# Optimization experiments

Hardware: AMD Instinct MI355X
Metric: run time of the kernel (lower is better)

## Reference

```python
import jax, jax.numpy as jnp
import numpy as np

T, H, I, E, K = 1024, 2048, 1408, 8, 2  # tokens, hidden, moe_intermediate, n_experts, top_k

def setup_inputs() -> dict:
    key = jax.random.key(0)
    k0, k1, k2, k3 = jax.random.split(key, 4)
    def w(k, shape, fan_in):
        return jax.random.normal(k, shape, jnp.float32) / np.float32(np.sqrt(fan_in))
    return {
        "hidden_states": jax.random.normal(k0, (T, H), jnp.float32),
        "gate_w": w(k1, (H, E), H),      # router: LiteLinear(H -> E), no bias
        "w1": w(k2, (E, H, I), H),        # experts_w1 [E, H, I]
        "w2": w(k3, (E, I, H), I),        # experts_w2 [E, I, H]
    }

def reference(hidden_states, gate_w, w1, w2):
    # Router: logits -> softmax -> top-k expert probabilities (no renorm; Qwen2MoE norm_topk_prob=False)
    router_logits = hidden_states @ gate_w                      # [T, E]
    probs = jax.nn.softmax(router_logits, axis=-1)              # [T, E]
    topk_vals, topk_idx = jax.lax.top_k(probs, K)               # [T, K]
    # Dense combine weights: zero except at the top-k experts of each token
    combine = jnp.sum(jax.nn.one_hot(topk_idx, E, dtype=probs.dtype) * topk_vals[..., None], axis=1)  # [T, E]
    # Expert MLP per source: down(silu(x @ w1)) — note: no gate/up split in this repo's fused_moe weights
    h = jnp.einsum('th,ehi->tei', hidden_states, w1)            # [T, E, I]
    y = jnp.einsum('tei,eih->teh', jax.nn.silu(h), w2)          # [T, E, H]
    return jnp.einsum('te,teh->th', combine, y)                 # [T, H]
```

## Files before the change

### kernel.cpp

```cpp
#include <hip/hip_runtime.h>
#include <hip/hip_fp16.h>

#define T_TOK 1024
#define H_DIM 2048
#define I_DIM 1408
#define N_EXP 8
#define TOPK  2

using f16x8 = __attribute__((ext_vector_type(8))) _Float16;
using f16x4 = __attribute__((ext_vector_type(4))) _Float16;
using f32x4 = __attribute__((ext_vector_type(4))) float;

#define BM 128
#define BN 64
#define BK 32
#define LDSP 40
#define NTHR 512

#define WS_COUNTS      0
#define WS_BASES       256
#define WS_CURSORS     512
#define WS_TOPK_E      768
#define WS_TOPK_W      (768 + 8192)
#define WS_TOK_OF_SLOT 17408
#define WS_W_OF_SLOT   29696
#define WS_HACT        43008
#define WS_NEEDED      (43008 + 8650752)

__global__ void k_zero_counts(int* counts) {
    if (threadIdx.x < N_EXP) counts[threadIdx.x] = 0;
}

__global__ void k_router(const float* __restrict__ X, const float* __restrict__ GW,
                         int* __restrict__ counts, int* __restrict__ topk_e,
                         float* __restrict__ topk_w) {
    int t = (blockIdx.x * blockDim.x + threadIdx.x) >> 6;
    int lane = threadIdx.x & 63;
    if (t >= T_TOK) return;
    float acc[N_EXP];
#pragma unroll
    for (int e = 0; e < N_EXP; ++e) acc[e] = 0.f;
    const float* xrow = X + (size_t)t * H_DIM;
    for (int h = lane; h < H_DIM; h += 64) {
        float x = xrow[h];
        const float* g = GW + (size_t)h * N_EXP;
#pragma unroll
        for (int e = 0; e < N_EXP; ++e) acc[e] = fmaf(x, g[e], acc[e]);
    }
#pragma unroll
    for (int off = 32; off > 0; off >>= 1) {
#pragma unroll
        for (int e = 0; e < N_EXP; ++e) acc[e] += __shfl_xor(acc[e], off, 64);
    }
    if (lane == 0) {
        float m = acc[0];
#pragma unroll
        for (int e = 1; e < N_EXP; ++e) m = fmaxf(m, acc[e]);
        float ex[N_EXP], s = 0.f;
#pragma unroll
        for (int e = 0; e < N_EXP; ++e) { ex[e] = expf(acc[e] - m); s += ex[e]; }
        float inv = 1.f / s;
        int e1 = 0;
#pragma unroll
        for (int e = 1; e < N_EXP; ++e) if (ex[e] > ex[e1]) e1 = e;
        int e2 = (e1 == 0) ? 1 : 0;
#pragma unroll
        for (int e = 0; e < N_EXP; ++e) if (e != e1 && ex[e] > ex[e2]) e2 = e;
        topk_e[t * 2 + 0] = e1;
        topk_e[t * 2 + 1] = e2;
        topk_w[t * 2 + 0] = ex[e1] * inv;
        topk_w[t * 2 + 1] = ex[e2] * inv;
        atomicAdd(&counts[e1], 1);
        atomicAdd(&counts[e2], 1);
    }
}

__global__ void k_prefix(const int* __restrict__ counts, int* __restrict__ bases,
                         int* __restrict__ cursors) {
    if (threadIdx.x == 0) {
        int b = 0;
        for (int e = 0; e < N_EXP; ++e) {
            bases[e] = b;
            b += ((counts[e] + BM - 1) / BM) * BM;
            cursors[e] = 0;
        }
    }
}

__global__ void k_scatter(const int* __restrict__ topk_e, const float* __restrict__ topk_w,
                          const int* __restrict__ bases, int* __restrict__ cursors,
                          int* __restrict__ tok_of_slot, float* __restrict__ w_of_slot) {
    int t = blockIdx.x * blockDim.x + threadIdx.x;
    if (t >= T_TOK) return;
    for (int j = 0; j < TOPK; ++j) {
        int e = topk_e[t * 2 + j];
        int pos = atomicAdd(&cursors[e], 1);
        int slot = bases[e] + pos;
        tok_of_slot[slot] = t;
        w_of_slot[slot] = topk_w[t * 2 + j];
    }
}

__global__ void k_zero_out(float* __restrict__ out) {
    int i = blockIdx.x * blockDim.x + threadIdx.x;
    ((float4*)out)[i] = float4{0.f, 0.f, 0.f, 0.f};
}

__global__ __launch_bounds__(NTHR) void k_gemm1(
    const float* __restrict__ X, const float* __restrict__ W1,
    const int* __restrict__ counts, const int* __restrict__ bases,
    const int* __restrict__ tok_of_slot, const float* __restrict__ w_of_slot,
    _Float16* __restrict__ hact) {
    __shared__ _Float16 As[2][BM][LDSP];
    __shared__ _Float16 Bs[2][BN][LDSP];

    const int e = blockIdx.z;
    const int cnt = counts[e];
    const int m0 = blockIdx.y * BM;
    if (m0 >= cnt) return;
    const int base = bases[e];
    const int n0 = blockIdx.x * BN;
    const int tid = threadIdx.x;

    const int ar = tid >> 2;
    const int akc = (tid & 3) * 8;
    const int r_eff = min(ar, cnt - m0 - 1);
    const float* arow = X + (size_t)tok_of_slot[base + m0 + r_eff] * H_DIM + akc;

    const int bn = tid & 63;
    const int bkq = (tid >> 6) * 4;
    const float* bcol = W1 + (size_t)e * H_DIM * I_DIM + (size_t)bkq * I_DIM + n0 + bn;

    const int wid = tid >> 6, lane = tid & 63;
    const int wm = (wid >> 1) * 32, wn = (wid & 1) * 32;
    const int rsel = lane & 15, ksel = (lane >> 4) * 8;

    f32x4 acc[2][2] = {};
    float a_reg[8], b_reg[4];

    auto load_regs = [&](int k0) {
        *(float4*)(a_reg + 0) = *(const float4*)(arow + k0);
        *(float4*)(a_reg + 4) = *(const float4*)(arow + k0 + 4);
        const float* bp = bcol + (size_t)k0 * I_DIM;
        b_reg[0] = bp[0];
        b_reg[1] = bp[I_DIM];
        b_reg[2] = bp[2 * I_DIM];
        b_reg[3] = bp[3 * I_DIM];
    };
    auto store_lds = [&](int buf) {
        f16x8 a;
#pragma unroll
        for (int j = 0; j < 8; ++j) a[j] = (_Float16)a_reg[j];
        *(f16x8*)&As[buf][ar][akc] = a;
        f16x4 b;
#pragma unroll
        for (int j = 0; j < 4; ++j) b[j] = (_Float16)b_reg[j];
        *(f16x4*)&Bs[buf][bn][bkq] = b;
    };

    load_regs(0);
    store_lds(0);
    __syncthreads();
    const int KT = H_DIM / BK;
    for (int kt = 0; kt < KT; ++kt) {
        const int cur = kt & 1;
        if (kt + 1 < KT) load_regs((kt + 1) * BK);
        f16x8 af[2], bf[2];
#pragma unroll
        for (int i = 0; i < 2; ++i)
            af[i] = *(const f16x8*)&As[cur][wm + i * 16 + rsel][ksel];
#pragma unroll
        for (int j = 0; j < 2; ++j)
            bf[j] = *(const f16x8*)&Bs[cur][wn + j * 16 + rsel][ksel];
#pragma unroll
        for (int i = 0; i < 2; ++i)
#pragma unroll
            for (int j = 0; j < 2; ++j)
                acc[i][j] = __builtin_amdgcn_mfma_f32_16x16x32_f16(af[i], bf[j], acc[i][j], 0, 0, 0);
        if (kt + 1 < KT) store_lds(cur ^ 1);
        __syncthreads();
    }

    const int rows = cnt - m0;
#pragma unroll
    for (int i = 0; i < 2; ++i) {
#pragma unroll
        for (int q = 0; q < 4; ++q) {
            int r = wm + i * 16 + (lane >> 4) * 4 + q;
            if (r < rows) {
                int slot = base + m0 + r;
                float w = w_of_slot[slot];
                _Float16* hrow = hact + (size_t)slot * I_DIM + n0;
#pragma unroll
                for (int j = 0; j < 2; ++j) {
                    float v = acc[i][j][q];
                    float s = v / (1.f + expf(-v)) * w;
                    hrow[wn + j * 16 + rsel] = (_Float16)s;
                }
            }
        }
    }
}

__global__ __launch_bounds__(NTHR) void k_gemm2(
    const _Float16* __restrict__ hact, const float* __restrict__ W2,
    const int* __restrict__ counts, const int* __restrict__ bases,
    const int* __restrict__ tok_of_slot, float* __restrict__ out) {
    __shared__ _Float16 As[2][BM][LDSP];
    __shared__ _Float16 Bs[2][BN][LDSP];

    const int e = blockIdx.z;
    const int cnt = counts[e];
    const int m0 = blockIdx.y * BM;
    if (m0 >= cnt) return;
    const int base = bases[e];
    const int n0 = blockIdx.x * BN;
    const int tid = threadIdx.x;

    const int ar = tid >> 2;
    const int akc = (tid & 3) * 8;
    const int r_eff = min(ar, cnt - m0 - 1);
    const _Float16* arow = hact + (size_t)(base + m0 + r_eff) * I_DIM + akc;

    const int bn = tid & 63;
    const int bkq = (tid >> 6) * 4;
    const float* bcol = W2 + (size_t)e * I_DIM * H_DIM + (size_t)bkq * H_DIM + n0 + bn;

    const int wid = tid >> 6, lane = tid & 63;
    const int wm = (wid >> 1) * 32, wn = (wid & 1) * 32;
    const int rsel = lane & 15, ksel = (lane >> 4) * 8;

    f32x4 acc[2][2] = {};
    f16x8 a_reg;
    float b_reg[4];

    auto load_regs = [&](int k0) {
        a_reg = *(const f16x8*)(arow + k0);
        const float* bp = bcol + (size_t)k0 * H_DIM;
        b_reg[0] = bp[0];
        b_reg[1] = bp[H_DIM];
        b_reg[2] = bp[2 * H_DIM];
        b_reg[3] = bp[3 * H_DIM];
    };
    auto store_lds = [&](int buf) {
        *(f16x8*)&As[buf][ar][akc] = a_reg;
        f16x4 b;
#pragma unroll
        for (int j = 0; j < 4; ++j) b[j] = (_Float16)b_reg[j];
        *(f16x4*)&Bs[buf][bn][bkq] = b;
    };

    load_regs(0);
    store_lds(0);
    __syncthreads();
    const int KT = I_DIM / BK;
    for (int kt = 0; kt < KT; ++kt) {
        const int cur = kt & 1;
        if (kt + 1 < KT) load_regs((kt + 1) * BK);
        f16x8 af[2], bf[2];
#pragma unroll
        for (int i = 0; i < 2; ++i)
            af[i] = *(const f16x8*)&As[cur][wm + i * 16 + rsel][ksel];
#pragma unroll
        for (int j = 0; j < 2; ++j)
            bf[j] = *(const f16x8*)&Bs[cur][wn + j * 16 + rsel][ksel];
#pragma unroll
        for (int i = 0; i < 2; ++i)
#pragma unroll
            for (int j = 0; j < 2; ++j)
                acc[i][j] = __builtin_amdgcn_mfma_f32_16x16x32_f16(af[i], bf[j], acc[i][j], 0, 0, 0);
        if (kt + 1 < KT) store_lds(cur ^ 1);
        __syncthreads();
    }

    const int rows = cnt - m0;
#pragma unroll
    for (int i = 0; i < 2; ++i) {
#pragma unroll
        for (int q = 0; q < 4; ++q) {
            int r = wm + i * 16 + (lane >> 4) * 4 + q;
            if (r < rows) {
                int slot = base + m0 + r;
                int tok = tok_of_slot[slot];
                float* orow = out + (size_t)tok * H_DIM + n0;
#pragma unroll
                for (int j = 0; j < 2; ++j)
                    atomicAdd(&orow[wn + j * 16 + rsel], acc[i][j][q]);
            }
        }
    }
}

extern "C" void kernel_launch(void* const* d_in, const int* in_sizes, int n_in,
                              void* d_out, int out_size, void* d_ws, size_t ws_size,
                              hipStream_t stream) {
    const float* X  = (const float*)d_in[0];
    const float* GW = (const float*)d_in[1];
    const float* W1 = (const float*)d_in[2];
    const float* W2 = (const float*)d_in[3];
    float* out = (float*)d_out;
    char* ws = (char*)d_ws;
    if (ws_size < (size_t)WS_NEEDED) return;

    int*   counts      = (int*)(ws + WS_COUNTS);
    int*   bases       = (int*)(ws + WS_BASES);
    int*   cursors     = (int*)(ws + WS_CURSORS);
    int*   topk_e      = (int*)(ws + WS_TOPK_E);
    float* topk_w      = (float*)(ws + WS_TOPK_W);
    int*   tok_of_slot = (int*)(ws + WS_TOK_OF_SLOT);
    float* w_of_slot   = (float*)(ws + WS_W_OF_SLOT);
    _Float16* hact     = (_Float16*)(ws + WS_HACT);

    k_zero_counts<<<1, 64, 0, stream>>>(counts);
    k_router<<<T_TOK / 4, 256, 0, stream>>>(X, GW, counts, topk_e, topk_w);
    k_prefix<<<1, 64, 0, stream>>>(counts, bases, cursors);
    k_scatter<<<T_TOK / 256, 256, 0, stream>>>(topk_e, topk_w, bases, cursors,
                                               tok_of_slot, w_of_slot);
    k_zero_out<<<(T_TOK * H_DIM / 4) / 256, 256, 0, stream>>>(out);
    k_gemm1<<<dim3(I_DIM / BN, T_TOK / BM, N_EXP), NTHR, 0, stream>>>(
        X, W1, counts, bases, tok_of_slot, w_of_slot, hact);
    k_gemm2<<<dim3(H_DIM / BN, T_TOK / BM, N_EXP), NTHR, 0, stream>>>(
        hact, W2, counts, bases, tok_of_slot, out);
}
```

Before: 193.9 us.

## Double K tile, XOR-swizzle LDS, register double-buffer prefetch in MoE GEMMs

Both expert GEMMs now use a K tile of 64 instead of 32, which halves the number of barriers per output tile. The padded LDS rows are replaced by an XOR swizzle to avoid bank conflicts. Two register sets are used to prefetch global loads two tiles ahead, and launch bounds now request 4 blocks per CU. The zeroing kernels are swapped for hipMemsetAsync. The cost is higher register pressure, which could spill under the occupancy hint.

```diff
diff --git a/kernel.cpp b/kernel.cpp
--- a/kernel.cpp
+++ b/kernel.cpp
@@ -8,13 +8,11 @@
 #define TOPK  2
 
 using f16x8 = __attribute__((ext_vector_type(8))) _Float16;
-using f16x4 = __attribute__((ext_vector_type(4))) _Float16;
 using f32x4 = __attribute__((ext_vector_type(4))) float;
 
 #define BM 128
 #define BN 64
-#define BK 32
-#define LDSP 40
+#define BK 64
 #define NTHR 512
 
 #define WS_COUNTS      0
@@ -26,10 +24,6 @@
 #define WS_W_OF_SLOT   29696
 #define WS_HACT        43008
 #define WS_NEEDED      (43008 + 8650752)
-
-__global__ void k_zero_counts(int* counts) {
-    if (threadIdx.x < N_EXP) counts[threadIdx.x] = 0;
-}
 
 __global__ void k_router(const float* __restrict__ X, const float* __restrict__ GW,
                          int* __restrict__ counts, int* __restrict__ topk_e,
@@ -101,18 +95,13 @@
     }
 }
 
-__global__ void k_zero_out(float* __restrict__ out) {
-    int i = blockIdx.x * blockDim.x + threadIdx.x;
-    ((float4*)out)[i] = float4{0.f, 0.f, 0.f, 0.f};
-}
-
-__global__ __launch_bounds__(NTHR) void k_gemm1(
+__global__ __launch_bounds__(NTHR, 4) void k_gemm1(
     const float* __restrict__ X, const float* __restrict__ W1,
     const int* __restrict__ counts, const int* __restrict__ bases,
     const int* __restrict__ tok_of_slot, const float* __restrict__ w_of_slot,
     _Float16* __restrict__ hact) {
-    __shared__ _Float16 As[2][BM][LDSP];
-    __shared__ _Float16 Bs[2][BN][LDSP];
+    __shared__ _Float16 As[2][BM][BK];
+    __shared__ _Float16 Bs[2][BN][BK];
 
     const int e = blockIdx.z;
     const int cnt = counts[e];
@@ -123,70 +112,96 @@
     const int tid = threadIdx.x;
 
     const int ar = tid >> 2;
-    const int akc = (tid & 3) * 8;
+    const int ac2 = (tid & 3) * 2;
     const int r_eff = min(ar, cnt - m0 - 1);
-    const float* arow = X + (size_t)tok_of_slot[base + m0 + r_eff] * H_DIM + akc;
+    const float* arow = X + (size_t)tok_of_slot[base + m0 + r_eff] * H_DIM + (tid & 3) * 16;
 
     const int bn = tid & 63;
-    const int bkq = (tid >> 6) * 4;
-    const float* bcol = W1 + (size_t)e * H_DIM * I_DIM + (size_t)bkq * I_DIM + n0 + bn;
+    const int bc = tid >> 6;
+    const float* bcol = W1 + (size_t)e * H_DIM * I_DIM + (size_t)(bc * 8) * I_DIM + n0 + bn;
 
     const int wid = tid >> 6, lane = tid & 63;
     const int wm = (wid >> 1) * 32, wn = (wid & 1) * 32;
-    const int rsel = lane & 15, ksel = (lane >> 4) * 8;
+    const int rsel = lane & 15, kq = lane >> 4;
 
     f32x4 acc[2][2] = {};
-    float a_reg[8], b_reg[4];
-
-    auto load_regs = [&](int k0) {
-        *(float4*)(a_reg + 0) = *(const float4*)(arow + k0);
-        *(float4*)(a_reg + 4) = *(const float4*)(arow + k0 + 4);
-        const float* bp = bcol + (size_t)k0 * I_DIM;
-        b_reg[0] = bp[0];
-        b_reg[1] = bp[I_DIM];
-        b_reg[2] = bp[2 * I_DIM];
-        b_reg[3] = bp[3 * I_DIM];
-    };
-    auto store_lds = [&](int buf) {
-        f16x8 a;
-#pragma unroll
-        for (int j = 0; j < 8; ++j) a[j] = (_Float16)a_reg[j];
-        *(f16x8*)&As[buf][ar][akc] = a;
-        f16x4 b;
-#pragma unroll
-        for (int j = 0; j < 4; ++j) b[j] = (_Float16)b_reg[j];
-        *(f16x4*)&Bs[buf][bn][bkq] = b;
-    };
-
-    load_regs(0);
-    store_lds(0);
+
+    float4 aR0[4]; float bR0[8];
+    float4 aR1[4]; float bR1[8];
+
+#define LOAD1(aR, bR, k0)                                              \
+    do {                                                               \
+        aR[0] = *(const float4*)(arow + (k0));                         \
+        aR[1] = *(const float4*)(arow + (k0) + 4);                     \
+        aR[2] = *(const float4*)(arow + (k0) + 8);                     \
+        aR[3] = *(const float4*)(arow + (k0) + 12);                    \
+        const float* bp = bcol + (size_t)(k0) * I_DIM;                 \
+        _Pragma("unroll") for (int j = 0; j < 8; ++j)                  \
+            bR[j] = bp[(size_t)j * I_DIM];                             \
+    } while (0)
+
+#define STORE1(buf, aR, bR)                                            \
+    do {                                                               \
+        f16x8 p0, p1;                                                  \
+        _Pragma("unroll") for (int j = 0; j < 4; ++j) {                \
+            p0[j]     = (_Float16)aR[0][j];                            \
+            p0[j + 4] = (_Float16)aR[1][j];                            \
+            p1[j]     = (_Float16)aR[2][j];                            \
+            p1[j + 4] = (_Float16)aR[3][j];                            \
+        }                                                              \
+        *(f16x8*)&As[buf][ar][((ac2) ^ (ar & 7)) * 8] = p0;            \
+        *(f16x8*)&As[buf][ar][((ac2 + 1) ^ (ar & 7)) * 8] = p1;        \
+        f16x8 q;                                                       \
+        _Pragma("unroll") for (int j = 0; j < 8; ++j)                  \
+            q[j] = (_Float16)bR[j];                                    \
+        *(f16x8*)&Bs[buf][bn][(bc ^ (bn & 7)) * 8] = q;                \
+    } while (0)
+
+#define COMPUTE(buf)                                                   \
+    do {                                                               \
+        _Pragma("unroll") for (int ks = 0; ks < 2; ++ks) {             \
+            f16x8 af[2], bf[2];                                        \
+            _Pragma("unroll") for (int i = 0; i < 2; ++i) {            \
+                int r = wm + i * 16 + rsel;                            \
+                af[i] = *(const f16x8*)&As[buf][r][((kq + 4 * ks) ^ (r & 7)) * 8]; \
+            }                                                          \
+            _Pragma("unroll") for (int j = 0; j < 2; ++j) {            \
+                int r = wn + j * 16 + rsel;                            \
+                bf[j] = *(const f16x8*)&Bs[buf][r][((kq + 4 * ks) ^ (r & 7)) * 8]; \
+            }                                                          \
+            _Pragma("unroll") for (int i = 0; i < 2; ++i)              \
+                _Pragma("unroll") for (int j = 0; j < 2; ++j)          \
+                    acc[i][j] = __builtin_amdgcn_mfma_f32_16x16x32_f16(af[i], bf[j], acc[i][j], 0, 0, 0); \
+        }                                                              \
+    } while (0)
+
+    const int KT = H_DIM / BK;
+    LOAD1(aR0, bR0, 0);
+    STORE1(0, aR0, bR0);
+    LOAD1(aR0, bR0, BK);
     __syncthreads();
-    const int KT = H_DIM / BK;
-    for (int kt = 0; kt < KT; ++kt) {
-        const int cur = kt & 1;
-        if (kt + 1 < KT) load_regs((kt + 1) * BK);
-        f16x8 af[2], bf[2];
-#pragma unroll
-        for (int i = 0; i < 2; ++i)
-            af[i] = *(const f16x8*)&As[cur][wm + i * 16 + rsel][ksel];
-#pragma unroll
-        for (int j = 0; j < 2; ++j)
-            bf[j] = *(const f16x8*)&Bs[cur][wn + j * 16 + rsel][ksel];
-#pragma unroll
-        for (int i = 0; i < 2; ++i)
-#pragma unroll
-            for (int j = 0; j < 2; ++j)
-                acc[i][j] = __builtin_amdgcn_mfma_f32_16x16x32_f16(af[i], bf[j], acc[i][j], 0, 0, 0);
-        if (kt + 1 < KT) store_lds(cur ^ 1);
+    for (int kt = 0; kt < KT; kt += 2) {
+        if (kt + 2 < KT) LOAD1(aR1, bR1, (kt + 2) * BK);
+        COMPUTE(0);
+        if (kt + 1 < KT) STORE1(1, aR0, bR0);
         __syncthreads();
-    }
+        if (kt + 3 < KT) LOAD1(aR0, bR0, (kt + 3) * BK);
+        if (kt + 1 < KT) {
+            COMPUTE(1);
+            if (kt + 2 < KT) STORE1(0, aR1, bR1);
+            __syncthreads();
+        }
+    }
+#undef LOAD1
+#undef STORE1
+#undef COMPUTE
 
     const int rows = cnt - m0;
 #pragma unroll
     for (int i = 0; i < 2; ++i) {
 #pragma unroll
         for (int q = 0; q < 4; ++q) {
-            int r = wm + i * 16 + (lane >> 4) * 4 + q;
+            int r = wm + i * 16 + kq * 4 + q;
             if (r < rows) {
                 int slot = base + m0 + r;
                 float w = w_of_slot[slot];
@@ -202,12 +217,12 @@
     }
 }
 
-__global__ __launch_bounds__(NTHR) void k_gemm2(
+__global__ __launch_bounds__(NTHR, 4) void k_gemm2(
     const _Float16* __restrict__ hact, const float* __restrict__ W2,
     const int* __restrict__ counts, const int* __restrict__ bases,
     const int* __restrict__ tok_of_slot, float* __restrict__ out) {
-    __shared__ _Float16 As[2][BM][LDSP];
-    __shared__ _Float16 Bs[2][BN][LDSP];
+    __shared__ _Float16 As[2][BM][BK];
+    __shared__ _Float16 Bs[2][BN][BK];
 
     const int e = blockIdx.z;
     const int cnt = counts[e];
@@ -218,67 +233,87 @@
     const int tid = threadIdx.x;
 
     const int ar = tid >> 2;
-    const int akc = (tid & 3) * 8;
+    const int ac2 = (tid & 3) * 2;
     const int r_eff = min(ar, cnt - m0 - 1);
-    const _Float16* arow = hact + (size_t)(base + m0 + r_eff) * I_DIM + akc;
+    const _Float16* arow = hact + (size_t)(base + m0 + r_eff) * I_DIM + (tid & 3) * 16;
 
     const int bn = tid & 63;
-    const int bkq = (tid >> 6) * 4;
-    const float* bcol = W2 + (size_t)e * I_DIM * H_DIM + (size_t)bkq * H_DIM + n0 + bn;
+    const int bc = tid >> 6;
+    const float* bcol = W2 + (size_t)e * I_DIM * H_DIM + (size_t)(bc * 8) * H_DIM + n0 + bn;
 
     const int wid = tid >> 6, lane = tid & 63;
     const int wm = (wid >> 1) * 32, wn = (wid & 1) * 32;
-    const int rsel = lane & 15, ksel = (lane >> 4) * 8;
+    const int rsel = lane & 15, kq = lane >> 4;
 
     f32x4 acc[2][2] = {};
-    f16x8 a_reg;
-    float b_reg[4];
-
-    auto load_regs = [&](int k0) {
-        a_reg = *(const f16x8*)(arow + k0);
-        const float* bp = bcol + (size_t)k0 * H_DIM;
-        b_reg[0] = bp[0];
-        b_reg[1] = bp[H_DIM];
-        b_reg[2] = bp[2 * H_DIM];
-        b_reg[3] = bp[3 * H_DIM];
-    };
-    auto store_lds = [&](int buf) {
-        *(f16x8*)&As[buf][ar][akc] = a_reg;
-        f16x4 b;
-#pragma unroll
-        for (int j = 0; j < 4; ++j) b[j] = (_Float16)b_reg[j];
-        *(f16x4*)&Bs[buf][bn][bkq] = b;
-    };
-
-    load_regs(0);
-    store_lds(0);
+
+    f16x8 aR0[2]; float bR0[8];
+    f16x8 aR1[2]; float bR1[8];
+
+#define LOAD2(aR, bR, k0)                                              \
+    do {                                                               \
+        aR[0] = *(const f16x8*)(arow + (k0));                          \
+        aR[1] = *(const f16x8*)(arow + (k0) + 8);                      \
+        const float* bp = bcol + (size_t)(k0) * H_DIM;                 \
+        _Pragma("unroll") for (int j = 0; j < 8; ++j)                  \
+            bR[j] = bp[(size_t)j * H_DIM];                             \
+    } while (0)
+
+#define STORE2(buf, aR, bR)                                            \
+    do {                                                               \
+        *(f16x8*)&As[buf][ar][((ac2) ^ (ar & 7)) * 8] = aR[0];         \
+        *(f16x8*)&As[buf][ar][((ac2 + 1) ^ (ar & 7)) * 8] = aR[1];     \
+        f16x8 q;                                                       \
+        _Pragma("unroll") for (int j = 0; j < 8; ++j)                  \
+            q[j] = (_Float16)bR[j];                                    \
+        *(f16x8*)&Bs[buf][bn][(bc ^ (bn & 7)) * 8] = q;                \
+    } while (0)
+
+#define COMPUTE2(buf)                                                  \
+    do {                                                               \
+        _Pragma("unroll") for (int ks = 0; ks < 2; ++ks) {             \
+            f16x8 af[2], bf[2];                                        \
+            _Pragma("unroll") for (int i = 0; i < 2; ++i) {            \
+                int r = wm + i * 16 + rsel;                            \
+                af[i] = *(const f16x8*)&As[buf][r][((kq + 4 * ks) ^ (r & 7)) * 8]; \
+            }                                                          \
+            _Pragma("unroll") for (int j = 0; j < 2; ++j) {            \
+                int r = wn + j * 16 + rsel;                            \
+                bf[j] = *(const f16x8*)&Bs[buf][r][((kq + 4 * ks) ^ (r & 7)) * 8]; \
+            }                                                          \
+            _Pragma("unroll") for (int i = 0; i < 2; ++i)              \
+                _Pragma("unroll") for (int j = 0; j < 2; ++j)          \
+                    acc[i][j] = __builtin_amdgcn_mfma_f32_16x16x32_f16(af[i], bf[j], acc[i][j], 0, 0, 0); \
+        }                                                              \
+    } while (0)
+
+    const int KT = I_DIM / BK;
+    LOAD2(aR0, bR0, 0);
+    STORE2(0, aR0, bR0);
+    LOAD2(aR0, bR0, BK);
     __syncthreads();
-    const int KT = I_DIM / BK;
-    for (int kt = 0; kt < KT; ++kt) {
-        const int cur = kt & 1;
-        if (kt + 1 < KT) load_regs((kt + 1) * BK);
-        f16x8 af[2], bf[2];
-#pragma unroll
-        for (int i = 0; i < 2; ++i)
-            af[i] = *(const f16x8*)&As[cur][wm + i * 16 + rsel][ksel];
-#pragma unroll
-        for (int j = 0; j < 2; ++j)
-            bf[j] = *(const f16x8*)&Bs[cur][wn + j * 16 + rsel][ksel];
-#pragma unroll
-        for (int i = 0; i < 2; ++i)
-#pragma unroll
-            for (int j = 0; j < 2; ++j)
-                acc[i][j] = __builtin_amdgcn_mfma_f32_16x16x32_f16(af[i], bf[j], acc[i][j], 0, 0, 0);
-        if (kt + 1 < KT) store_lds(cur ^ 1);
+    for (int kt = 0; kt < KT; kt += 2) {
+        if (kt + 2 < KT) LOAD2(aR1, bR1, (kt + 2) * BK);
+        COMPUTE2(0);
+        if (kt + 1 < KT) STORE2(1, aR0, bR0);
         __syncthreads();
-    }
+        if (kt + 3 < KT) LOAD2(aR0, bR0, (kt + 3) * BK);
+        if (kt + 1 < KT) {
+            COMPUTE2(1);
+            if (kt + 2 < KT) STORE2(0, aR1, bR1);
+            __syncthreads();
+        }
+    }
+#undef LOAD2
+#undef STORE2
+#undef COMPUTE2
 
     const int rows = cnt - m0;
 #pragma unroll
     for (int i = 0; i < 2; ++i) {
 #pragma unroll
         for (int q = 0; q < 4; ++q) {
-            int r = wm + i * 16 + (lane >> 4) * 4 + q;
+            int r = wm + i * 16 + kq * 4 + q;
             if (r < rows) {
                 int slot = base + m0 + r;
                 int tok = tok_of_slot[slot];
@@ -311,12 +346,12 @@
     float* w_of_slot   = (float*)(ws + WS_W_OF_SLOT);
     _Float16* hact     = (_Float16*)(ws + WS_HACT);
 
-    k_zero_counts<<<1, 64, 0, stream>>>(counts);
+    hipMemsetAsync(counts, 0, N_EXP * sizeof(int), stream);
     k_router<<<T_TOK / 4, 256, 0, stream>>>(X, GW, counts, topk_e, topk_w);
     k_prefix<<<1, 64, 0, stream>>>(counts, bases, cursors);
     k_scatter<<<T_TOK / 256, 256, 0, stream>>>(topk_e, topk_w, bases, cursors,
                                                tok_of_slot, w_of_slot);
-    k_zero_out<<<(T_TOK * H_DIM / 4) / 256, 256, 0, stream>>>(out);
+    hipMemsetAsync(out, 0, (size_t)T_TOK * H_DIM * sizeof(float), stream);
     k_gemm1<<<dim3(I_DIM / BN, T_TOK / BM, N_EXP), NTHR, 0, stream>>>(
         X, W1, counts, bases, tok_of_slot, w_of_slot, hact);
     k_gemm2<<<dim3(H_DIM / BN, T_TOK / BM, N_EXP), NTHR, 0, stream>>>(
```

Result: faster. 166.1 us (-14.3%).
